# Optimization experiments

Hardware: AMD Instinct MI355X
Metric: run time of the kernel (lower is better)

Reference implementation:

```python
import jax, jax.numpy as jnp
import numpy as np

HID = 1024
HEADS = 16
HEAD_DIM = HID // HEADS
NEG = -10000000000.0


def setup_inputs() -> dict:
    key = jax.random.key(0)
    ks = jax.random.split(key, 12)
    B, S = 4, 2048
    scale = 1.0 / np.sqrt(HID)
    inp = {
        "query": jax.random.normal(ks[0], (B, S, HID), dtype=jnp.float32),
        "key": jax.random.normal(ks[1], (B, S, HID), dtype=jnp.float32),
        "value": jax.random.normal(ks[2], (B, S, HID), dtype=jnp.float32),
        "Wq": jax.random.normal(ks[3], (HID, HID), dtype=jnp.float32) * scale,
        "bq": jnp.zeros((HID,), dtype=jnp.float32),
        "Wk": jax.random.normal(ks[4], (HID, HID), dtype=jnp.float32) * scale,
        "bk": jnp.zeros((HID,), dtype=jnp.float32),
        "Wv": jax.random.normal(ks[5], (HID, HID), dtype=jnp.float32) * scale,
        "bv": jnp.zeros((HID,), dtype=jnp.float32),
        "Wo": jax.random.normal(ks[6], (HID, HID), dtype=jnp.float32) * scale,
        "bo": jnp.zeros((HID,), dtype=jnp.float32),
    }
    return inp


def reference(query, key, value, Wq, bq, Wk, bk, Wv, bv, Wo, bo):
    B, S, _ = query.shape
    # linear projections (nn.Linear: x @ W.T + b)
    q = query @ Wq.T + bq
    k = key @ Wk.T + bk
    v = value @ Wv.T + bv
    # split heads -> [B, H, S, D]
    q = q.reshape(B, S, HEADS, HEAD_DIM).transpose(0, 2, 1, 3)
    k = k.reshape(B, S, HEADS, HEAD_DIM).transpose(0, 2, 1, 3)
    v = v.reshape(B, S, HEADS, HEAD_DIM).transpose(0, 2, 1, 3)
    # NOTE: original module computes self.scale but never applies it -> unscaled logits
    attn = jnp.einsum("bhqd,bhkd->bhqk", q, k)
    causal = jnp.tril(jnp.ones((S, S), dtype=bool))
    attn = jnp.where(causal, attn, NEG)
    attn = jax.nn.softmax(attn, axis=-1)
    x = jnp.einsum("bhqk,bhkd->bhqd", attn, v)
    x = x.transpose(0, 2, 1, 3).reshape(B, S, HID)
    return x @ Wo.T + bo
```

## Files before the change

### kernel.cpp

```cpp
#include <hip/hip_runtime.h>
#include <hip/hip_fp16.h>

typedef _Float16 half_t;
typedef half_t halfx8 __attribute__((ext_vector_type(8)));
typedef half_t halfx4 __attribute__((ext_vector_type(4)));
typedef float floatx4 __attribute__((ext_vector_type(4)));

#define HID 1024
#define HEADS 16
#define HD 64
#define BATCH 4
#define SEQ 2048
#define MTOT (BATCH * SEQ)
#define NWELEM (HID * HID)

#define MFMA_F16 __builtin_amdgcn_mfma_f32_16x16x32_f16

__device__ inline halfx8 load8h(const half_t* p) { return *(const halfx8*)p; }
__device__ inline halfx8 load8h(const float* p) {
    floatx4 x = *(const floatx4*)p;
    floatx4 y = *(const floatx4*)(p + 4);
    halfx8 r;
    r[0] = (half_t)x[0]; r[1] = (half_t)x[1];
    r[2] = (half_t)x[2]; r[3] = (half_t)x[3];
    r[4] = (half_t)y[0]; r[5] = (half_t)y[1];
    r[6] = (half_t)y[2]; r[7] = (half_t)y[3];
    return r;
}

__device__ __forceinline__ uint32_t pack2h(float a, float b) {
    union { half_t h[2]; uint32_t u; } r;
    r.h[0] = (half_t)a; r.h[1] = (half_t)b;
    return r.u;
}

__device__ __forceinline__ void gl_lds16(const half_t* g, half_t* lds) {
    __builtin_amdgcn_global_load_lds(
        (const __attribute__((address_space(1))) void*)g,
        (__attribute__((address_space(3))) void*)lds, 16, 0, 0);
}

template <int MODE, typename TOut>
__device__ __forceinline__ void epilogue_store(
    const floatx4 (&acc)[4][4], const float* __restrict__ bias,
    TOut* __restrict__ Out, int m0, int n0, int wm, int wn, int quad, int l16)
{
    float bvals[4];
#pragma unroll
    for (int nt = 0; nt < 4; ++nt)
        bvals[nt] = bias[n0 + wn + nt * 16 + l16];

#pragma unroll
    for (int mt = 0; mt < 4; ++mt) {
        const int mbase = m0 + wm + mt * 16 + quad * 4;
#pragma unroll
        for (int nt = 0; nt < 4; ++nt) {
            const int n = n0 + wn + nt * 16 + l16;
            if (MODE == 2) {
                const int b = mbase >> 11, s = mbase & (SEQ - 1);
                const int h = n >> 6, d = n & (HD - 1);
                halfx4 st;
#pragma unroll
                for (int r = 0; r < 4; ++r)
                    st[r] = (half_t)(acc[mt][nt][r] + bvals[nt]);
                *(halfx4*)((half_t*)Out +
                    ((((size_t)b * HEADS + h) * HD + d) << 11) + s) = st;
            } else {
#pragma unroll
                for (int r = 0; r < 4; ++r) {
                    const float v = acc[mt][nt][r] + bvals[nt];
                    const int mm  = mbase + r;
                    if (MODE == 0) {
                        const int b = mm >> 11, s = mm & (SEQ - 1);
                        const int h = n >> 6, d = n & (HD - 1);
                        Out[((((size_t)b * HEADS + h) * SEQ + s) << 6) + d] = (TOut)v;
                    } else {
                        Out[(size_t)mm * HID + n] = (TOut)v;
                    }
                }
            }
        }
    }
}

template <int MODE, typename TOut>
__global__ __launch_bounds__(256) void gemm16(
    const half_t* __restrict__ A, const half_t* __restrict__ W,
    const float* __restrict__ bias, TOut* __restrict__ Out)
{
    __shared__ half_t As[2][128 * 32];
    __shared__ half_t Bs[2][128 * 32];

    const int tid  = threadIdx.x;
    const int id   = blockIdx.y * gridDim.x + blockIdx.x;
    const int cpx  = (gridDim.x * gridDim.y) >> 3;
    const int swz  = (id & 7) * cpx + (id >> 3);
    const int m0   = (swz >> 3) * 128;
    const int n0   = (swz & 7) * 128;
    const int wave = tid >> 6;
    const int lane = tid & 63;
    const int quad = lane >> 4;
    const int l16  = lane & 15;
    const int wm   = (wave >> 1) * 64;
    const int wn   = (wave & 1) * 64;

    const int c0   = wave * 2;
    const int srow = c0 * 16 + (lane >> 2);
    const int scol = (lane & 3) * 8;
    const half_t* aptr0 = A + (size_t)(m0 + srow) * HID + scol;
    const half_t* aptr1 = aptr0 + (size_t)16 * HID;
    const half_t* bptr0 = W + (size_t)(n0 + srow) * HID + scol;
    const half_t* bptr1 = bptr0 + (size_t)16 * HID;

    floatx4 acc[4][4];
    const floatx4 zero4 = {0.f, 0.f, 0.f, 0.f};
#pragma unroll
    for (int mt = 0; mt < 4; ++mt)
#pragma unroll
        for (int nt = 0; nt < 4; ++nt) acc[mt][nt] = zero4;

    auto stage = [&](int buf, int k0) {
        gl_lds16(aptr0 + k0, &As[buf][c0 * 512]);
        gl_lds16(aptr1 + k0, &As[buf][c0 * 512 + 512]);
        gl_lds16(bptr0 + k0, &Bs[buf][c0 * 512]);
        gl_lds16(bptr1 + k0, &Bs[buf][c0 * 512 + 512]);
    };
    auto compute = [&](int buf) {
        halfx8 af[4], bfr[4];
#pragma unroll
        for (int t = 0; t < 4; ++t) {
            af[t]  = *(const halfx8*)&As[buf][(wm + t * 16 + l16) * 32 + quad * 8];
            bfr[t] = *(const halfx8*)&Bs[buf][(wn + t * 16 + l16) * 32 + quad * 8];
        }
#pragma unroll
        for (int mt = 0; mt < 4; ++mt)
#pragma unroll
            for (int nt = 0; nt < 4; ++nt)
                acc[mt][nt] = MFMA_F16(af[mt], bfr[nt], acc[mt][nt], 0, 0, 0);
    };

    stage(0, 0);
    __syncthreads();
    for (int k0 = 0; k0 < HID; k0 += 64) {
        stage(1, k0 + 32);
        compute(0);
        __syncthreads();
        if (k0 + 64 < HID) stage(0, k0 + 64);
        compute(1);
        __syncthreads();
    }

    epilogue_store<MODE, TOut>(acc, bias, Out, m0, n0, wm, wn, quad, l16);
}

template <int MODE, typename TA, typename TOut>
__global__ __launch_bounds__(256) void gemm_bt(
    const TA* __restrict__ A, const float* __restrict__ W,
    const float* __restrict__ bias, TOut* __restrict__ Out)
{
    __shared__ half_t As[128][40];
    __shared__ half_t Bs[128][40];

    const int tid  = threadIdx.x;
    const int m0   = blockIdx.y * 128;
    const int n0   = blockIdx.x * 128;
    const int wave = tid >> 6;
    const int lane = tid & 63;
    const int quad = lane >> 4;
    const int l16  = lane & 15;
    const int wm   = (wave >> 1) * 64;
    const int wn   = (wave & 1) * 64;
    const int trow = tid >> 1;
    const int tcol = (tid & 1) * 16;

    const TA*    aptr = A + (size_t)(m0 + trow) * HID + tcol;
    const float* bptr = W + (size_t)(n0 + trow) * HID + tcol;

    floatx4 acc[4][4];
    const floatx4 zero4 = {0.f, 0.f, 0.f, 0.f};
#pragma unroll
    for (int mt = 0; mt < 4; ++mt)
#pragma unroll
        for (int nt = 0; nt < 4; ++nt) acc[mt][nt] = zero4;

    for (int k0 = 0; k0 < HID; k0 += 32) {
        halfx8 av0 = load8h(aptr);
        halfx8 av1 = load8h(aptr + 8);
        halfx8 bv0 = load8h(bptr);
        halfx8 bv1 = load8h(bptr + 8);
        aptr += 32;
        bptr += 32;

        __syncthreads();
        *(halfx8*)&As[trow][tcol]     = av0;
        *(halfx8*)&As[trow][tcol + 8] = av1;
        *(halfx8*)&Bs[trow][tcol]     = bv0;
        *(halfx8*)&Bs[trow][tcol + 8] = bv1;
        __syncthreads();

        halfx8 af[4], bfr[4];
#pragma unroll
        for (int t = 0; t < 4; ++t) {
            af[t]  = *(const halfx8*)&As[wm + t * 16 + l16][quad * 8];
            bfr[t] = *(const halfx8*)&Bs[wn + t * 16 + l16][quad * 8];
        }
#pragma unroll
        for (int mt = 0; mt < 4; ++mt)
#pragma unroll
            for (int nt = 0; nt < 4; ++nt)
                acc[mt][nt] = MFMA_F16(af[mt], bfr[nt], acc[mt][nt], 0, 0, 0);
    }

    epilogue_store<MODE, TOut>(acc, bias, Out, m0, n0, wm, wn, quad, l16);
}

__global__ __launch_bounds__(256) void cvt_act(
    const float* __restrict__ in, half_t* __restrict__ out)
{
    const size_t i = ((size_t)blockIdx.x * 256 + threadIdx.x) * 8;
    *(halfx8*)(out + i) = load8h(in + i);
}

__global__ __launch_bounds__(256) void cvt_w4(
    const float* __restrict__ w0, const float* __restrict__ w1,
    const float* __restrict__ w2, const float* __restrict__ w3,
    half_t* __restrict__ out)
{
    const int t = blockIdx.y;
    const float* src = (t == 0) ? w0 : (t == 1) ? w1 : (t == 2) ? w2 : w3;
    const size_t i = ((size_t)blockIdx.x * 256 + threadIdx.x) * 8;
    *(halfx8*)(out + (size_t)t * NWELEM + i) = load8h(src + i);
}

__global__ __launch_bounds__(256) void attn_kernel(
    const half_t* __restrict__ Q, const half_t* __restrict__ K,
    const half_t* __restrict__ VT, half_t* __restrict__ O)
{
    __shared__ half_t Ks[64][72];
    __shared__ half_t Vt[64][72];

    const int bh  = blockIdx.x;
    const int qt  = (gridDim.y - 1) - blockIdx.y;
    const int q0  = qt * 128;
    const int tid = threadIdx.x;
    const int wave = tid >> 6;
    const int lane = tid & 63;
    const int quad = lane >> 4;
    const int l16  = lane & 15;

    const half_t* Qb  = Q  + (size_t)bh * SEQ * HD;
    const half_t* Kb  = K  + (size_t)bh * SEQ * HD;
    const half_t* VTb = VT + (size_t)bh * HD * SEQ;

    halfx8 aq[2][2];
#pragma unroll
    for (int mt = 0; mt < 2; ++mt) {
        const half_t* p = Qb + (size_t)(q0 + wave * 32 + mt * 16 + l16) * HD + quad * 8;
        aq[mt][0] = *(const halfx8*)p;
        aq[mt][1] = *(const halfx8*)(p + 32);
    }

    const floatx4 zero4 = {0.f, 0.f, 0.f, 0.f};
    floatx4 oaccT[2][4];
    float mrow[2], lrow[2];
#pragma unroll
    for (int mt = 0; mt < 2; ++mt) {
        mrow[mt] = -3.0e38f;
        lrow[mt] = 0.f;
#pragma unroll
        for (int dt = 0; dt < 4; ++dt) oaccT[mt][dt] = zero4;
    }

    const int srow = tid >> 2;
    const int scol = (tid & 3) * 16;
    const int ktiles = 2 * qt + 2;

    union U8 { halfx8 h; uint32_t u[4]; };

    halfx8 nk0, nk1, nv0, nv1;
    {
        const half_t* ksrc = Kb + (size_t)srow * HD + scol;
        nk0 = *(const halfx8*)ksrc;
        nk1 = *(const halfx8*)(ksrc + 8);
        const half_t* vsrc = VTb + (size_t)srow * SEQ + scol;
        nv0 = *(const halfx8*)vsrc;
        nv1 = *(const halfx8*)(vsrc + 8);
    }

    for (int kt = 0; kt < ktiles; ++kt) {
        const int k0 = kt * 64;
        __syncthreads();
        *(halfx8*)&Ks[srow][scol]     = nk0;
        *(halfx8*)&Ks[srow][scol + 8] = nk1;
        *(halfx8*)&Vt[srow][scol]     = nv0;
        *(halfx8*)&Vt[srow][scol + 8] = nv1;
        __syncthreads();

        if (kt + 1 < ktiles) {
            const int kn = k0 + 64;
            const half_t* ksrc = Kb + (size_t)(kn + srow) * HD + scol;
            nk0 = *(const halfx8*)ksrc;
            nk1 = *(const halfx8*)(ksrc + 8);
            const half_t* vsrc = VTb + (size_t)srow * SEQ + kn + scol;
            nv0 = *(const halfx8*)vsrc;
            nv1 = *(const halfx8*)(vsrc + 8);
        }

        const bool active = (k0 <= q0 + wave * 32 + 31);

        if (active) {
            floatx4 sacc[2][4];
#pragma unroll
            for (int mt = 0; mt < 2; ++mt)
#pragma unroll
                for (int nt = 0; nt < 4; ++nt) sacc[mt][nt] = zero4;
#pragma unroll
            for (int nt = 0; nt < 4; ++nt) {
                halfx8 bk0 = *(const halfx8*)&Ks[nt * 16 + l16][quad * 8];
                halfx8 bk1 = *(const halfx8*)&Ks[nt * 16 + l16][quad * 8 + 32];
#pragma unroll
                for (int mt = 0; mt < 2; ++mt) {
                    sacc[mt][nt] = MFMA_F16(bk0, aq[mt][0], sacc[mt][nt], 0, 0, 0);
                    sacc[mt][nt] = MFMA_F16(bk1, aq[mt][1], sacc[mt][nt], 0, 0, 0);
                }
            }

            if (kt >= 2 * qt) {
#pragma unroll
                for (int mt = 0; mt < 2; ++mt) {
                    const int qg = q0 + wave * 32 + mt * 16 + l16;
#pragma unroll
                    for (int nt = 0; nt < 4; ++nt) {
                        const int kg = k0 + nt * 16 + quad * 4;
#pragma unroll
                        for (int r = 0; r < 4; ++r)
                            if (kg + r > qg) sacc[mt][nt][r] = -1.0e30f;
                    }
                }
            }

            uint32_t pk[2][4][2];
#pragma unroll
            for (int mt = 0; mt < 2; ++mt) {
                float mx = sacc[mt][0][0];
#pragma unroll
                for (int nt = 0; nt < 4; ++nt)
#pragma unroll
                    for (int r = 0; r < 4; ++r)
                        if (nt | r) mx = fmaxf(mx, sacc[mt][nt][r]);
                mx = fmaxf(mx, __shfl_xor(mx, 16));
                mx = fmaxf(mx, __shfl_xor(mx, 32));

                if (!__all(mx <= mrow[mt] + 8.f)) {
                    const float mnew  = fmaxf(mrow[mt], mx);
                    const float alpha = __expf(mrow[mt] - mnew);
                    mrow[mt] = mnew;
                    lrow[mt] *= alpha;
#pragma unroll
                    for (int dt = 0; dt < 4; ++dt) oaccT[mt][dt] *= alpha;
                }

                float rsum = 0.f;
#pragma unroll
                for (int nt = 0; nt < 4; ++nt)
#pragma unroll
                    for (int r = 0; r < 4; ++r) {
                        const float p = __expf(sacc[mt][nt][r] - mrow[mt]);
                        sacc[mt][nt][r] = p;
                        rsum += p;
                    }
#pragma unroll
                for (int nt = 0; nt < 4; ++nt) {
                    pk[mt][nt][0] = pack2h(sacc[mt][nt][0], sacc[mt][nt][1]);
                    pk[mt][nt][1] = pack2h(sacc[mt][nt][2], sacc[mt][nt][3]);
                }
                rsum += __shfl_xor(rsum, 16);
                rsum += __shfl_xor(rsum, 32);
                lrow[mt] += rsum;
            }

            U8 pb[2][2];
#pragma unroll
            for (int mt = 0; mt < 2; ++mt)
#pragma unroll
                for (int s2 = 0; s2 < 2; ++s2)
#pragma unroll
                    for (int w = 0; w < 4; ++w) {
                        const int src = l16 + ((quad & 1) << 5) + ((w >> 1) << 4);
                        const uint32_t lo =
                            (uint32_t)__shfl((int)pk[mt][2 * s2][w & 1], src, 64);
                        const uint32_t hi =
                            (uint32_t)__shfl((int)pk[mt][2 * s2 + 1][w & 1], src, 64);
                        pb[mt][s2].u[w] = (quad >> 1) ? hi : lo;
                    }

#pragma unroll
            for (int s2 = 0; s2 < 2; ++s2)
#pragma unroll
                for (int dt = 0; dt < 4; ++dt) {
                    halfx8 bv = *(const halfx8*)&Vt[dt * 16 + l16][s2 * 32 + quad * 8];
                    oaccT[0][dt] = MFMA_F16(bv, pb[0][s2].h, oaccT[0][dt], 0, 0, 0);
                    oaccT[1][dt] = MFMA_F16(bv, pb[1][s2].h, oaccT[1][dt], 0, 0, 0);
                }
        }
    }

    const int b = bh >> 4, h = bh & (HEADS - 1);
#pragma unroll
    for (int mt = 0; mt < 2; ++mt) {
        const int q = q0 + wave * 32 + mt * 16 + l16;
#pragma unroll
        for (int dt = 0; dt < 4; ++dt) {
            halfx4 st;
#pragma unroll
            for (int r = 0; r < 4; ++r)
                st[r] = (half_t)(oaccT[mt][dt][r] / lrow[mt]);
            *(halfx4*)(O + (size_t)(b * SEQ + q) * HID +
                       h * HD + dt * 16 + quad * 4) = st;
        }
    }
}

extern "C" void kernel_launch(void* const* d_in, const int* in_sizes, int n_in,
                              void* d_out, int out_size, void* d_ws, size_t ws_size,
                              hipStream_t stream)
{
    const float* query = (const float*)d_in[0];
    const float* key   = (const float*)d_in[1];
    const float* value = (const float*)d_in[2];
    const float* Wq    = (const float*)d_in[3];
    const float* bq    = (const float*)d_in[4];
    const float* Wk    = (const float*)d_in[5];
    const float* bk    = (const float*)d_in[6];
    const float* Wv    = (const float*)d_in[7];
    const float* bv    = (const float*)d_in[8];
    const float* Wo    = (const float*)d_in[9];
    const float* bo    = (const float*)d_in[10];
    float* out = (float*)d_out;

    const size_t NE = (size_t)MTOT * HID;
    half_t* Qp  = (half_t*)d_ws;
    half_t* Kp  = Qp  + NE;
    half_t* VpT = Kp  + NE;
    half_t* Ob  = VpT + NE;
    half_t* W16 = Ob  + NE;
    const size_t need = (4 * NE + 4 * (size_t)NWELEM) * sizeof(half_t);

    dim3 gg(HID / 128, MTOT / 128);
    dim3 ga(BATCH * HEADS, SEQ / 128);

    if (ws_size >= need) {
        half_t* act16 = Ob;
        const unsigned actBlocks = (unsigned)(NE / 2048);
        const unsigned wBlocks   = (unsigned)(NWELEM / 2048);

        cvt_w4<<<dim3(wBlocks, 4), 256, 0, stream>>>(Wq, Wk, Wv, Wo, W16);

        cvt_act<<<actBlocks, 256, 0, stream>>>(query, act16);
        gemm16<0, half_t><<<gg, 256, 0, stream>>>(act16, W16, bq, Qp);
        cvt_act<<<actBlocks, 256, 0, stream>>>(key, act16);
        gemm16<0, half_t><<<gg, 256, 0, stream>>>(act16, W16 + NWELEM, bk, Kp);
        cvt_act<<<actBlocks, 256, 0, stream>>>(value, act16);
        gemm16<2, half_t><<<gg, 256, 0, stream>>>(act16, W16 + 2 * (size_t)NWELEM, bv, VpT);

        attn_kernel<<<ga, 256, 0, stream>>>(Qp, Kp, VpT, Ob);

        gemm16<1, float><<<gg, 256, 0, stream>>>(Ob, W16 + 3 * (size_t)NWELEM, bo, out);
    } else {
        gemm_bt<0, float, half_t><<<gg, 256, 0, stream>>>(query, Wq, bq, Qp);
        gemm_bt<0, float, half_t><<<gg, 256, 0, stream>>>(key,   Wk, bk, Kp);
        gemm_bt<2, float, half_t><<<gg, 256, 0, stream>>>(value, Wv, bv, VpT);
        attn_kernel<<<ga, 256, 0, stream>>>(Qp, Kp, VpT, Ob);
        gemm_bt<1, half_t, float><<<gg, 256, 0, stream>>>(Ob, Wo, bo, out);
    }
}
```

Measured before the change: 364.9 us.

## Widen GEMM K-tile to 64 with XOR-swizzled LDS and batch activation conversion

The fp16 GEMM now stages 128x64 K-slices per buffer instead of 128x32. Reads go through an XOR swizzle on the column slot to avoid LDS bank conflicts, which halves the number of barriers per K loop. The three activation conversions are merged into one launch, using the output buffer as scratch for two of the fp16 copies. This raises LDS use to 64 KB per block, which may limit occupancy, and it relies on the output buffer being large enough to hold scratch data.

```diff
diff --git a/kernel.cpp b/kernel.cpp
--- a/kernel.cpp
+++ b/kernel.cpp
@@ -83,14 +83,14 @@
     }
 }
 
-template <int MODE, typename TOut>
-__global__ __launch_bounds__(256) void gemm16(
+struct GemmCtx { int m0, n0, wm, wn, quad, l16; };
+
+template <typename EPI>
+__device__ __forceinline__ void gemm_body(
     const half_t* __restrict__ A, const half_t* __restrict__ W,
-    const float* __restrict__ bias, TOut* __restrict__ Out)
-{
-    __shared__ half_t As[2][128 * 32];
-    __shared__ half_t Bs[2][128 * 32];
-
+    half_t* As, half_t* Bs,
+    EPI&& epi)
+{
     const int tid  = threadIdx.x;
     const int id   = blockIdx.y * gridDim.x + blockIdx.x;
     const int cpx  = (gridDim.x * gridDim.y) >> 3;
@@ -104,13 +104,11 @@
     const int wm   = (wave >> 1) * 64;
     const int wn   = (wave & 1) * 64;
 
-    const int c0   = wave * 2;
-    const int srow = c0 * 16 + (lane >> 2);
-    const int scol = (lane & 3) * 8;
-    const half_t* aptr0 = A + (size_t)(m0 + srow) * HID + scol;
-    const half_t* aptr1 = aptr0 + (size_t)16 * HID;
-    const half_t* bptr0 = W + (size_t)(n0 + srow) * HID + scol;
-    const half_t* bptr1 = bptr0 + (size_t)16 * HID;
+    const int r8   = lane >> 3;
+    const int slot = (lane & 7) ^ r8;
+    const int srow = wave * 32 + r8;
+    const half_t* aP = A + (size_t)(m0 + srow) * HID + slot * 8;
+    const half_t* bP = W + (size_t)(n0 + srow) * HID + slot * 8;
 
     floatx4 acc[4][4];
     const floatx4 zero4 = {0.f, 0.f, 0.f, 0.f};
@@ -120,37 +118,62 @@
         for (int nt = 0; nt < 4; ++nt) acc[mt][nt] = zero4;
 
     auto stage = [&](int buf, int k0) {
-        gl_lds16(aptr0 + k0, &As[buf][c0 * 512]);
-        gl_lds16(aptr1 + k0, &As[buf][c0 * 512 + 512]);
-        gl_lds16(bptr0 + k0, &Bs[buf][c0 * 512]);
-        gl_lds16(bptr1 + k0, &Bs[buf][c0 * 512 + 512]);
+#pragma unroll
+        for (int c = 0; c < 4; ++c) {
+            gl_lds16(aP + (size_t)(8 * c) * HID + k0,
+                     &As[buf * 8192 + (wave * 32 + 8 * c) * 64]);
+            gl_lds16(bP + (size_t)(8 * c) * HID + k0,
+                     &Bs[buf * 8192 + (wave * 32 + 8 * c) * 64]);
+        }
     };
     auto compute = [&](int buf) {
-        halfx8 af[4], bfr[4];
-#pragma unroll
-        for (int t = 0; t < 4; ++t) {
-            af[t]  = *(const halfx8*)&As[buf][(wm + t * 16 + l16) * 32 + quad * 8];
-            bfr[t] = *(const halfx8*)&Bs[buf][(wn + t * 16 + l16) * 32 + quad * 8];
-        }
-#pragma unroll
-        for (int mt = 0; mt < 4; ++mt)
-#pragma unroll
-            for (int nt = 0; nt < 4; ++nt)
-                acc[mt][nt] = MFMA_F16(af[mt], bfr[nt], acc[mt][nt], 0, 0, 0);
+#pragma unroll
+        for (int ks = 0; ks < 2; ++ks) {
+            halfx8 af[4], bfr[4];
+#pragma unroll
+            for (int t = 0; t < 4; ++t) {
+                const int ra = wm + t * 16 + l16;
+                af[t]  = *(const halfx8*)&As[buf * 8192 + ra * 64 +
+                          ((ks * 32 + quad * 8) ^ ((ra & 7) << 3))];
+                const int rb = wn + t * 16 + l16;
+                bfr[t] = *(const halfx8*)&Bs[buf * 8192 + rb * 64 +
+                          ((ks * 32 + quad * 8) ^ ((rb & 7) << 3))];
+            }
+#pragma unroll
+            for (int mt = 0; mt < 4; ++mt)
+#pragma unroll
+                for (int nt = 0; nt < 4; ++nt)
+                    acc[mt][nt] = MFMA_F16(af[mt], bfr[nt], acc[mt][nt], 0, 0, 0);
+        }
     };
 
     stage(0, 0);
     __syncthreads();
-    for (int k0 = 0; k0 < HID; k0 += 64) {
-        stage(1, k0 + 32);
+    for (int k0 = 0; k0 < HID; k0 += 128) {
+        stage(1, k0 + 64);
         compute(0);
         __syncthreads();
-        if (k0 + 64 < HID) stage(0, k0 + 64);
+        if (k0 + 128 < HID) stage(0, k0 + 128);
         compute(1);
         __syncthreads();
     }
 
-    epilogue_store<MODE, TOut>(acc, bias, Out, m0, n0, wm, wn, quad, l16);
+    GemmCtx c{m0, n0, wm, wn, quad, l16};
+    epi(acc, c);
+}
+
+template <int MODE, typename TOut>
+__global__ __launch_bounds__(256) void gemm16(
+    const half_t* __restrict__ A, const half_t* __restrict__ W,
+    const float* __restrict__ bias, TOut* __restrict__ Out)
+{
+    __shared__ half_t As[2 * 128 * 64];
+    __shared__ half_t Bs[2 * 128 * 64];
+    gemm_body(A, W, As, Bs,
+        [&](const floatx4 (&acc)[4][4], const GemmCtx& c) {
+            epilogue_store<MODE, TOut>(acc, bias, Out, c.m0, c.n0,
+                                       c.wm, c.wn, c.quad, c.l16);
+        });
 }
 
 template <int MODE, typename TA, typename TOut>
@@ -214,11 +237,16 @@
     epilogue_store<MODE, TOut>(acc, bias, Out, m0, n0, wm, wn, quad, l16);
 }
 
-__global__ __launch_bounds__(256) void cvt_act(
-    const float* __restrict__ in, half_t* __restrict__ out)
-{
+__global__ __launch_bounds__(256) void cvt_act3(
+    const float* __restrict__ q, const float* __restrict__ k,
+    const float* __restrict__ v,
+    half_t* __restrict__ q16, half_t* __restrict__ k16, half_t* __restrict__ v16)
+{
+    const int t = blockIdx.y;
+    const float* src = (t == 0) ? q : (t == 1) ? k : v;
+    half_t* dst = (t == 0) ? q16 : (t == 1) ? k16 : v16;
     const size_t i = ((size_t)blockIdx.x * 256 + threadIdx.x) * 8;
-    *(halfx8*)(out + i) = load8h(in + i);
+    *(halfx8*)(dst + i) = load8h(src + i);
 }
 
 __global__ __launch_bounds__(256) void cvt_w4(
@@ -449,19 +477,20 @@
     dim3 gg(HID / 128, MTOT / 128);
     dim3 ga(BATCH * HEADS, SEQ / 128);
 
-    if (ws_size >= need) {
-        half_t* act16 = Ob;
+    if (ws_size >= need && (size_t)out_size >= 2 * NE * sizeof(half_t)) {
+        half_t* q16 = (half_t*)out;
+        half_t* k16 = q16 + NE;
+        half_t* v16 = Ob;
         const unsigned actBlocks = (unsigned)(NE / 2048);
         const unsigned wBlocks   = (unsigned)(NWELEM / 2048);
 
         cvt_w4<<<dim3(wBlocks, 4), 256, 0, stream>>>(Wq, Wk, Wv, Wo, W16);
-
-        cvt_act<<<actBlocks, 256, 0, stream>>>(query, act16);
-        gemm16<0, half_t><<<gg, 256, 0, stream>>>(act16, W16, bq, Qp);
-        cvt_act<<<actBlocks, 256, 0, stream>>>(key, act16);
-        gemm16<0, half_t><<<gg, 256, 0, stream>>>(act16, W16 + NWELEM, bk, Kp);
-        cvt_act<<<actBlocks, 256, 0, stream>>>(value, act16);
-        gemm16<2, half_t><<<gg, 256, 0, stream>>>(act16, W16 + 2 * (size_t)NWELEM, bv, VpT);
+        cvt_act3<<<dim3(actBlocks, 3), 256, 0, stream>>>(
+            query, key, value, q16, k16, v16);
+
+        gemm16<0, half_t><<<gg, 256, 0, stream>>>(q16, W16, bq, Qp);
+        gemm16<0, half_t><<<gg, 256, 0, stream>>>(k16, W16 + NWELEM, bk, Kp);
+        gemm16<2, half_t><<<gg, 256, 0, stream>>>(v16, W16 + 2 * (size_t)NWELEM, bv, VpT);
 
         attn_kernel<<<ga, 256, 0, stream>>>(Qp, Kp, VpT, Ob);
 
```

After: 434.2 us. 1.19x slower.
